# Performance work log

Measured on AMD Instinct MI355X. Metric: run time of the kernel, lower is better.

## Reference

```python
import jax, jax.numpy as jnp
import numpy as np

N_EMBD = 1024
N_HEADS = 16
HEAD_EMBD = N_EMBD // N_HEADS  # 64
TOTAL = N_HEADS * HEAD_EMBD


def setup_inputs() -> dict:
    key = jax.random.key(0)
    k_x, k_wqkv, k_bqkv, k_wo, k_bo = jax.random.split(key, 5)
    B, S = 2, 2048
    x = jax.random.normal(k_x, (B, S, N_EMBD), dtype=jnp.float32)
    # torch nn.Linear: weight (out, in), y = x @ W.T + b
    lim_qkv = 1.0 / np.sqrt(N_EMBD)
    W_qkv = jax.random.uniform(k_wqkv, (3 * TOTAL, N_EMBD), minval=-lim_qkv, maxval=lim_qkv, dtype=jnp.float32)
    b_qkv = jax.random.uniform(k_bqkv, (3 * TOTAL,), minval=-lim_qkv, maxval=lim_qkv, dtype=jnp.float32)
    lim_o = 1.0 / np.sqrt(TOTAL)
    W_out = jax.random.uniform(k_wo, (N_EMBD, TOTAL), minval=-lim_o, maxval=lim_o, dtype=jnp.float32)
    b_out = jax.random.uniform(k_bo, (N_EMBD,), minval=-lim_o, maxval=lim_o, dtype=jnp.float32)
    return {"x": x, "W_qkv": W_qkv, "b_qkv": b_qkv, "W_out": W_out, "b_out": b_out}


def reference(x, W_qkv, b_qkv, W_out, b_out):
    B, S, _ = x.shape
    qkv = x @ W_qkv.T + b_qkv  # (B, S, 3*H*E)
    # rearrange 'b s (t h e) -> t b h s e'
    qkv = qkv.reshape(B, S, 3, N_HEADS, HEAD_EMBD)
    q = jnp.transpose(qkv[:, :, 0], (0, 2, 1, 3))  # (B, H, S, E)
    k = jnp.transpose(qkv[:, :, 1], (0, 2, 1, 3))
    v = jnp.transpose(qkv[:, :, 2], (0, 2, 1, 3))
    scores = jnp.einsum('bhse,bhte->bhst', q, k) / jnp.sqrt(jnp.float32(HEAD_EMBD))
    # original: tril(scores) + triu(-10000, k=1) == strict-upper entries exactly -10000
    row = jnp.arange(S)[:, None]
    col = jnp.arange(S)[None, :]
    masked = jnp.where(col > row, jnp.float32(-10000.0), scores)
    attn = jax.nn.softmax(masked, axis=-1)  # (B, H, S, S)
    z = jnp.einsum('bhrc,bhce->bhre', attn, v)  # (B, H, S, E)
    z = jnp.transpose(z, (0, 2, 1, 3)).reshape(B, S, TOTAL)
    out = z @ W_out.T + b_out
    return (out, attn)
```

## Files before the change

### kernel.cpp

```cpp
#include <hip/hip_runtime.h>
#include <stdint.h>

typedef __attribute__((ext_vector_type(4))) float f32x4;
typedef __attribute__((ext_vector_type(8))) short short8v;
typedef __attribute__((ext_vector_type(4))) unsigned short ushort4v;

#define DEV __device__ __forceinline__
#define EXP2 __builtin_amdgcn_exp2f
#define WAITVM0 asm volatile("s_waitcnt vmcnt(0)" ::: "memory")
#define WAITVM2 asm volatile("s_waitcnt vmcnt(2)" ::: "memory")
#define WAITVM4 asm volatile("s_waitcnt vmcnt(4)" ::: "memory")
#define FENCE   asm volatile("" ::: "memory")
#define BARRIER __builtin_amdgcn_s_barrier()

DEV unsigned short f2bf(float x) {
    union { float f; uint32_t u; } v; v.f = x;
    uint32_t r = v.u + 0x7fffu + ((v.u >> 16) & 1u);
    return (unsigned short)(r >> 16);
}
DEV float bf2f(unsigned short h) {
    union { uint32_t u; float f; } v; v.u = ((uint32_t)h) << 16;
    return v.f;
}
DEV uint32_t cvtpk(float lo, float hi) {
    uint32_t r;
    asm("v_cvt_pk_bf16_f32 %0, %1, %2" : "=v"(r) : "v"(lo), "v"(hi));
    return r;
}
DEV f32x4 mfma16(short8v a, short8v b, f32x4 c) {
    return __builtin_amdgcn_mfma_f32_16x16x32_bf16(a, b, c, 0, 0, 0);
}
DEV void gload16(const unsigned short* g, unsigned short* l) {
    __builtin_amdgcn_global_load_lds(
        (const __attribute__((address_space(1))) unsigned int*)g,
        (__attribute__((address_space(3))) unsigned int*)l, 16, 0, 0);
}

__global__ void k_cvt3(const float* __restrict__ a, unsigned short* __restrict__ oa, int na4,
                       const float* __restrict__ b, unsigned short* __restrict__ ob, int nb4,
                       const float* __restrict__ c, unsigned short* __restrict__ oc, int nc4) {
    int i = blockIdx.x * blockDim.x + threadIdx.x;
    const float* in; unsigned short* out; int idx;
    if (i < na4) { in = a; out = oa; idx = i; }
    else if (i < na4 + nb4) { in = b; out = ob; idx = i - na4; }
    else { idx = i - na4 - nb4; if (idx >= nc4) return; in = c; out = oc; }
    f32x4 v = *(const f32x4*)(in + (size_t)idx * 4);
    ushort4v h;
#pragma unroll
    for (int j = 0; j < 4; ++j) h[j] = f2bf(v[j]);
    *(ushort4v*)(out + (size_t)idx * 4) = h;
}

template <int KDIM>
DEV void gemm_core(const unsigned short* __restrict__ APTR,
                   const unsigned short* __restrict__ BPTR,
                   f32x4 (&acc)[4][4]) {
    __shared__ __align__(16) unsigned short As[2][128 * 32], Bs[2][128 * 32];
    int tid = threadIdx.x, lane = tid & 63, w = tid >> 6;
    int bm = blockIdx.x, bn = blockIdx.y;
    int wr = (w >> 1) * 64, wc = (w & 1) * 64;
    int lrow = lane & 15, lseg = lane >> 4;
#pragma unroll
    for (int m = 0; m < 4; ++m)
#pragma unroll
        for (int n = 0; n < 4; ++n) acc[m][n] = (f32x4){0.f, 0.f, 0.f, 0.f};
    auto STAGE = [&](int buf, int k0) {
#pragma unroll
        for (int i = 0; i < 2; ++i) {
            int ch = i * 256 + tid;
            int row = ch >> 2, seg = ch & 3;
            gload16(APTR + (size_t)(bm * 128 + row) * KDIM + k0 + seg * 8,
                    &As[buf][(i * 256 + (tid & ~63)) * 8]);
            gload16(BPTR + (size_t)(bn * 128 + row) * KDIM + k0 + seg * 8,
                    &Bs[buf][(i * 256 + (tid & ~63)) * 8]);
        }
    };
    const int NT = KDIM / 32;
    STAGE(0, 0);
    for (int t = 0; t < NT; ++t) {
        if (t < NT - 1) { STAGE((t + 1) & 1, (t + 1) * 32); WAITVM4; } else WAITVM0;
        BARRIER;
        const unsigned short* as = As[t & 1];
        const unsigned short* bs = Bs[t & 1];
        short8v fa[4], fb[4];
#pragma unroll
        for (int m = 0; m < 4; ++m) {
            fa[m] = *(const short8v*)(as + (wr + m * 16 + lrow) * 32 + lseg * 8);
            fb[m] = *(const short8v*)(bs + (wc + m * 16 + lrow) * 32 + lseg * 8);
        }
#pragma unroll
        for (int m = 0; m < 4; ++m)
#pragma unroll
            for (int n = 0; n < 4; ++n)
                acc[m][n] = mfma16(fa[m], fb[n], acc[m][n]);
        FENCE; BARRIER;
    }
}

__global__ __launch_bounds__(256) void k_gemm_qkv(
    const unsigned short* __restrict__ XB, const unsigned short* __restrict__ WB,
    const float* __restrict__ BIAS, unsigned short* __restrict__ QKVB) {
    f32x4 acc[4][4];
    gemm_core<1024>(XB, WB, acc);
    int tid = threadIdx.x, lane = tid & 63, w = tid >> 6;
    int bm = blockIdx.x, bn = blockIdx.y;
    int wr = (w >> 1) * 64, wc = (w & 1) * 64;
    int lrow = lane & 15, lseg = lane >> 4;
    const int N = 3072;
#pragma unroll
    for (int n = 0; n < 4; ++n) {
        int col = bn * 128 + wc + n * 16 + lrow;
        float bv = BIAS[col];
#pragma unroll
        for (int m = 0; m < 4; ++m) {
            int row = bm * 128 + wr + m * 16 + lseg * 4;
#pragma unroll
            for (int i = 0; i < 4; ++i)
                QKVB[(size_t)(row + i) * N + col] = f2bf(acc[m][n][i] + bv);
        }
    }
}

__global__ __launch_bounds__(256) void k_gemm_out(
    const unsigned short* __restrict__ ZB, const unsigned short* __restrict__ WOB,
    const float* __restrict__ BIAS, float* __restrict__ OUT) {
    f32x4 acc[4][4];
    gemm_core<1024>(ZB, WOB, acc);
    int tid = threadIdx.x, lane = tid & 63, w = tid >> 6;
    int bm = blockIdx.x, bn = blockIdx.y;
    int wr = (w >> 1) * 64, wc = (w & 1) * 64;
    int lrow = lane & 15, lseg = lane >> 4;
    const int N = 1024;
#pragma unroll
    for (int n = 0; n < 4; ++n) {
        int col = bn * 128 + wc + n * 16 + lrow;
        float bv = BIAS[col];
#pragma unroll
        for (int m = 0; m < 4; ++m) {
            int row = bm * 128 + wr + m * 16 + lseg * 4;
#pragma unroll
            for (int i = 0; i < 4; ++i)
                OUT[(size_t)(row + i) * N + col] = acc[m][n][i] + bv;
        }
    }
}

__global__ void k_prep_v(const unsigned short* __restrict__ QKVB, unsigned short* __restrict__ VT) {
    __shared__ unsigned short vt[32][72];
    int bh = blockIdx.y, b = bh >> 4, h = bh & 15;
    int c0 = blockIdx.x * 32;
    int t = threadIdx.x;
    int c = t >> 3, e8 = (t & 7) * 8;
    *(short8v*)&vt[c][e8] =
        *(const short8v*)(QKVB + (size_t)(b * 2048 + c0 + c) * 3072 + 2048 + h * 64 + e8);
    __syncthreads();
    int e = t & 63, cg = t >> 6;
    unsigned short tmp[8];
#pragma unroll
    for (int i = 0; i < 8; ++i) tmp[i] = vt[cg * 8 + i][e];
    *(short8v*)(VT + ((size_t)bh * 64 + e) * 2048 + c0 + cg * 8) = *(short8v*)tmp;
}

__global__ __launch_bounds__(512) void k_attn(
    const unsigned short* __restrict__ QKVB, const unsigned short* __restrict__ VT,
    float* __restrict__ ATTN, unsigned short* __restrict__ Z) {
    __shared__ __align__(16) unsigned short KV[2][8192];
    __shared__ __align__(16) float Pl[8][16][68];

    const float SCALE = 0.18033688011112042f;
    int blk = blockIdx.x;
    int bh = blk & 31;
    int rtp = blk >> 5;
    int rt = (rtp < 8) ? (15 - rtp) : (rtp - 8);
    int b = bh >> 4, h = bh & 15;
    int tid = threadIdx.x, lane = tid & 63, w = tid >> 6;
    int lrow = lane & 15, lseg = lane >> 4;
    int r0 = rt * 128 + w * 16;
    int T = 2 * rt + 2;
    int Tw = (r0 >> 6) + 1;

    short8v qf[2];
    {
        const unsigned short* qp =
            QKVB + (size_t)(b * 2048 + r0 + lrow) * 3072 + h * 64 + lseg * 8;
#pragma unroll
        for (int kc = 0; kc < 2; ++kc) {
            short8v qr = *(const short8v*)(qp + kc * 32);
            short8v qs;
#pragma unroll
            for (int j = 0; j < 8; ++j)
                qs[j] = (short)f2bf(bf2f((unsigned short)qr[j]) * SCALE);
            qf[kc] = qs;
        }
    }

    auto STAGEKA = [&](int buf, int t) {
        const size_t kbase = ((size_t)b * 2048 + (size_t)t * 128) * 3072 + 1024 + h * 64;
#pragma unroll
        for (int i2 = 0; i2 < 2; ++i2) {
            int ch = i2 * 512 + tid;
            int c = ch >> 3, u = ch & 7, us = u ^ (c & 7);
            gload16(QKVB + kbase + (size_t)c * 3072 + us * 8,
                    &KV[buf][(i2 * 512 + (tid & ~63)) * 8]);
        }
    };
    float ls4[4] = {0.f, 0.f, 0.f, 0.f};
    int TA = rt + 1;
    STAGEKA(0, 0);
    for (int t = 0; t < TA; ++t) {
        if (t < TA - 1) { STAGEKA((t + 1) & 1, t + 1); WAITVM2; } else WAITVM0;
        BARRIER;
        const unsigned short* kb = KV[t & 1];
        f32x4 sc[8];
#pragma unroll
        for (int g = 0; g < 8; ++g) sc[g] = (f32x4){0.f, 0.f, 0.f, 0.f};
#pragma unroll
        for (int kc = 0; kc < 2; ++kc) {
            int uoff = (((kc * 4 + lseg) ^ (lrow & 7)) << 3);
#pragma unroll
            for (int g = 0; g < 8; ++g) {
                short8v kf = *(const short8v*)(kb + (g * 16 + lrow) * 64 + uoff);
                sc[g] = mfma16(qf[kc], kf, sc[g]);
            }
        }
        if (t < TA - 1) {
#pragma unroll
            for (int g = 0; g < 8; ++g)
#pragma unroll
                for (int i = 0; i < 4; ++i) ls4[i] += EXP2(sc[g][i]);
        } else {
            int c0 = t * 128;
#pragma unroll
            for (int g = 0; g < 8; ++g)
#pragma unroll
                for (int i = 0; i < 4; ++i) {
                    float sv = (c0 + g * 16 + lrow > r0 + lseg * 4 + i) ? -1e30f : sc[g][i];
                    ls4[i] += EXP2(sv);
                }
        }
        FENCE; BARRIER;
    }
#pragma unroll
    for (int off = 1; off < 16; off <<= 1)
#pragma unroll
        for (int i = 0; i < 4; ++i) ls4[i] += __shfl_xor(ls4[i], off, 64);
    float invl[4];
#pragma unroll
    for (int i = 0; i < 4; ++i) invl[i] = 1.0f / ls4[i];

    auto STAGEKB = [&](int buf, int t) {
        const size_t kbase = ((size_t)b * 2048 + (size_t)t * 64) * 3072 + 1024 + h * 64;
        int c = tid >> 3, u = tid & 7, us = u ^ (c & 7);
        gload16(QKVB + kbase + (size_t)c * 3072 + us * 8, &KV[buf][(tid & ~63) * 8]);
    };
    auto STAGEVB = [&](int buf, int t) {
        const size_t vbase = (size_t)bh * 64 * 2048 + (size_t)t * 64;
        int e = tid >> 3, u = tid & 7, us = u ^ (e & 7);
        gload16(VT + vbase + (size_t)e * 2048 + us * 8, &KV[buf][4096 + (tid & ~63) * 8]);
    };

    float* ab = ATTN + ((size_t)bh * 2048 + r0) * 2048;
    f32x4 zacc[4];
#pragma unroll
    for (int i = 0; i < 4; ++i) zacc[i] = (f32x4){0.f, 0.f, 0.f, 0.f};

    STAGEKB(0, 0); STAGEVB(0, 0);
    for (int t = 0; t < T; ++t) {
        if (t < T - 1) { STAGEKB((t + 1) & 1, t + 1); STAGEVB((t + 1) & 1, t + 1); WAITVM2; }
        else WAITVM0;
        BARRIER;
        if (t < Tw) {
            const unsigned short* kb = KV[t & 1];
            const unsigned short* vb = KV[t & 1] + 4096;
            int c0 = t * 64;
            f32x4 sc[4];
#pragma unroll
            for (int g = 0; g < 4; ++g) sc[g] = (f32x4){0.f, 0.f, 0.f, 0.f};
#pragma unroll
            for (int kc = 0; kc < 2; ++kc) {
                int uoff = (((kc * 4 + lseg) ^ (lrow & 7)) << 3);
#pragma unroll
                for (int g = 0; g < 4; ++g) {
                    short8v kf = *(const short8v*)(kb + (g * 16 + lrow) * 64 + uoff);
                    sc[g] = mfma16(qf[kc], kf, sc[g]);
                }
            }
            if (t < Tw - 1) {
#pragma unroll
                for (int g = 0; g < 4; ++g)
#pragma unroll
                    for (int i = 0; i < 4; ++i)
                        Pl[w][lseg * 4 + i][g * 16 + lrow] = EXP2(sc[g][i]) * invl[i];
            } else {
#pragma unroll
                for (int g = 0; g < 4; ++g)
#pragma unroll
                    for (int i = 0; i < 4; ++i) {
                        float sv = (c0 + g * 16 + lrow > r0 + lseg * 4 + i) ? -1e30f : sc[g][i];
                        Pl[w][lseg * 4 + i][g * 16 + lrow] = EXP2(sv) * invl[i];
                    }
            }
            short8v pf[2];
#pragma unroll
            for (int kc = 0; kc < 2; ++kc) {
                f32x4 p0 = *(const f32x4*)&Pl[w][lrow][kc * 32 + lseg * 8];
                f32x4 p1 = *(const f32x4*)&Pl[w][lrow][kc * 32 + lseg * 8 + 4];
                union { uint32_t u[4]; short8v s; } pu;
                pu.u[0] = cvtpk(p0[0], p0[1]);
                pu.u[1] = cvtpk(p0[2], p0[3]);
                pu.u[2] = cvtpk(p1[0], p1[1]);
                pu.u[3] = cvtpk(p1[2], p1[3]);
                pf[kc] = pu.s;
            }
#pragma unroll
            for (int kc = 0; kc < 2; ++kc) {
                int uoff = (((kc * 4 + lseg) ^ (lrow & 7)) << 3);
#pragma unroll
                for (int et = 0; et < 4; ++et) {
                    short8v vf = *(const short8v*)(vb + (et * 16 + lrow) * 64 + uoff);
                    zacc[et] = mfma16(pf[kc], vf, zacc[et]);
                }
            }
            {
                int row4 = lane >> 4, cq = lane & 15;
#pragma unroll
                for (int r4 = 0; r4 < 4; ++r4) {
                    int row = r4 * 4 + row4;
                    *(f32x4*)(ab + (size_t)row * 2048 + c0 + cq * 4) =
                        *(const f32x4*)(&Pl[w][row][cq * 4]);
                }
            }
        }
        FENCE; BARRIER;
    }

#pragma unroll
    for (int et = 0; et < 4; ++et)
#pragma unroll
        for (int i = 0; i < 4; ++i)
            Z[(size_t)(b * 2048 + r0 + lseg * 4 + i) * 1024 + h * 64 + et * 16 + lrow] =
                f2bf(zacc[et][i]);

    int czw = Tw * 64;
    const f32x4 zz = (f32x4){0.f, 0.f, 0.f, 0.f};
    for (int r = 0; r < 16; ++r) {
        float* rp = ab + (size_t)r * 2048;
        for (int c = czw + (lane << 2); c < 2048; c += 256)
            *(f32x4*)(rp + c) = zz;
    }
}

extern "C" void kernel_launch(void* const* d_in, const int* in_sizes, int n_in,
                              void* d_out, int out_size, void* d_ws, size_t ws_size,
                              hipStream_t stream) {
    const float* X    = (const float*)d_in[0];
    const float* Wqkv = (const float*)d_in[1];
    const float* Bqkv = (const float*)d_in[2];
    const float* Wout = (const float*)d_in[3];
    const float* Bout = (const float*)d_in[4];
    float* out  = (float*)d_out;
    float* attn = out + (size_t)4096 * 1024;

    char* ws = (char*)d_ws;
    unsigned short* QKVB = (unsigned short*)ws; ws += (size_t)4096 * 3072 * 2;
    unsigned short* VTp  = (unsigned short*)ws; ws += (size_t)32 * 64 * 2048 * 2;
    unsigned short* ZBp  = (unsigned short*)ws; ws += (size_t)4096 * 1024 * 2;
    unsigned short* XBp  = (unsigned short*)ws; ws += (size_t)4096 * 1024 * 2;
    unsigned short* WQBp = (unsigned short*)ws; ws += (size_t)3072 * 1024 * 2;
    unsigned short* WOBp = (unsigned short*)ws; ws += (size_t)1024 * 1024 * 2;

    const int na4 = 4096 * 1024 / 4, nb4 = 3072 * 1024 / 4, nc4 = 1024 * 1024 / 4;
    k_cvt3<<<(na4 + nb4 + nc4 + 255) / 256, 256, 0, stream>>>(
        X, XBp, na4, Wqkv, WQBp, nb4, Wout, WOBp, nc4);
    k_gemm_qkv<<<dim3(32, 24), 256, 0, stream>>>(XBp, WQBp, Bqkv, QKVB);
    k_prep_v<<<dim3(64, 32), 256, 0, stream>>>(QKVB, VTp);
    k_attn<<<512, 512, 0, stream>>>(QKVB, VTp, attn, ZBp);
    k_gemm_out<<<dim3(32, 8), 256, 0, stream>>>(ZBp, WOBp, Bout, out);
}
```

Baseline: 243.4 us.

## Specialize warps in pass A: half compute row sums, half zero-fill masked attention

During the first (row-sum) pass, warps 0-3 now each compute softmax denominators for 32 rows, reusing staged K tiles across two Q fragments. Warps 4-7 meanwhile write zeros to the fully masked upper-triangle region of the attention output, interleaved across the pass-A iterations. Reciprocal sums are shared through shared memory. The intent is to hide the large zero-fill store traffic behind pass-A compute instead of doing it at the end, at the cost of halving the MFMA warps in pass A. A launch-bounds occupancy hint is also added.

```diff
diff --git a/kernel.cpp b/kernel.cpp
--- a/kernel.cpp
+++ b/kernel.cpp
@@ -10,6 +10,7 @@
 #define WAITVM0 asm volatile("s_waitcnt vmcnt(0)" ::: "memory")
 #define WAITVM2 asm volatile("s_waitcnt vmcnt(2)" ::: "memory")
 #define WAITVM4 asm volatile("s_waitcnt vmcnt(4)" ::: "memory")
+#define WAITLGKM0 asm volatile("s_waitcnt lgkmcnt(0)" ::: "memory")
 #define FENCE   asm volatile("" ::: "memory")
 #define BARRIER __builtin_amdgcn_s_barrier()
 
@@ -161,11 +162,12 @@
     *(short8v*)(VT + ((size_t)bh * 64 + e) * 2048 + c0 + cg * 8) = *(short8v*)tmp;
 }
 
-__global__ __launch_bounds__(512) void k_attn(
+__global__ __launch_bounds__(512, 4) void k_attn(
     const unsigned short* __restrict__ QKVB, const unsigned short* __restrict__ VT,
     float* __restrict__ ATTN, unsigned short* __restrict__ Z) {
     __shared__ __align__(16) unsigned short KV[2][8192];
     __shared__ __align__(16) float Pl[8][16][68];
+    __shared__ float Rinv[128];
 
     const float SCALE = 0.18033688011112042f;
     int blk = blockIdx.x;
@@ -178,6 +180,7 @@
     int r0 = rt * 128 + w * 16;
     int T = 2 * rt + 2;
     int Tw = (r0 >> 6) + 1;
+    int TA = rt + 1;
 
     short8v qf[2];
     {
@@ -197,56 +200,100 @@
     auto STAGEKA = [&](int buf, int t) {
         const size_t kbase = ((size_t)b * 2048 + (size_t)t * 128) * 3072 + 1024 + h * 64;
 #pragma unroll
-        for (int i2 = 0; i2 < 2; ++i2) {
-            int ch = i2 * 512 + tid;
+        for (int i2 = 0; i2 < 4; ++i2) {
+            int ch = i2 * 256 + tid;
             int c = ch >> 3, u = ch & 7, us = u ^ (c & 7);
             gload16(QKVB + kbase + (size_t)c * 3072 + us * 8,
-                    &KV[buf][(i2 * 512 + (tid & ~63)) * 8]);
+                    &KV[buf][(i2 * 256 + (tid & ~63)) * 8]);
         }
     };
-    float ls4[4] = {0.f, 0.f, 0.f, 0.f};
-    int TA = rt + 1;
-    STAGEKA(0, 0);
-    for (int t = 0; t < TA; ++t) {
-        if (t < TA - 1) { STAGEKA((t + 1) & 1, t + 1); WAITVM2; } else WAITVM0;
-        BARRIER;
-        const unsigned short* kb = KV[t & 1];
-        f32x4 sc[8];
-#pragma unroll
-        for (int g = 0; g < 8; ++g) sc[g] = (f32x4){0.f, 0.f, 0.f, 0.f};
-#pragma unroll
-        for (int kc = 0; kc < 2; ++kc) {
-            int uoff = (((kc * 4 + lseg) ^ (lrow & 7)) << 3);
-#pragma unroll
-            for (int g = 0; g < 8; ++g) {
-                short8v kf = *(const short8v*)(kb + (g * 16 + lrow) * 64 + uoff);
-                sc[g] = mfma16(qf[kc], kf, sc[g]);
-            }
-        }
-        if (t < TA - 1) {
-#pragma unroll
-            for (int g = 0; g < 8; ++g)
-#pragma unroll
-                for (int i = 0; i < 4; ++i) ls4[i] += EXP2(sc[g][i]);
-        } else {
-            int c0 = t * 128;
-#pragma unroll
-            for (int g = 0; g < 8; ++g)
-#pragma unroll
-                for (int i = 0; i < 4; ++i) {
-                    float sv = (c0 + g * 16 + lrow > r0 + lseg * 4 + i) ? -1e30f : sc[g][i];
-                    ls4[i] += EXP2(sv);
+    const f32x4 zz = (f32x4){0.f, 0.f, 0.f, 0.f};
+
+    if (w < 4) {
+        int r0A = rt * 128 + w * 32;
+        short8v qa[2][2];
+#pragma unroll
+        for (int g2 = 0; g2 < 2; ++g2) {
+            const unsigned short* qp =
+                QKVB + (size_t)(b * 2048 + r0A + g2 * 16 + lrow) * 3072 + h * 64 + lseg * 8;
+#pragma unroll
+            for (int kc = 0; kc < 2; ++kc) {
+                short8v qr = *(const short8v*)(qp + kc * 32);
+                short8v qs;
+#pragma unroll
+                for (int j = 0; j < 8; ++j)
+                    qs[j] = (short)f2bf(bf2f((unsigned short)qr[j]) * SCALE);
+                qa[g2][kc] = qs;
+            }
+        }
+        float ls8[8] = {0.f, 0.f, 0.f, 0.f, 0.f, 0.f, 0.f, 0.f};
+        STAGEKA(0, 0);
+        for (int t = 0; t < TA; ++t) {
+            if (t < TA - 1) { STAGEKA((t + 1) & 1, t + 1); WAITVM4; } else WAITVM0;
+            BARRIER;
+            const unsigned short* kb = KV[t & 1];
+#pragma unroll
+            for (int g2 = 0; g2 < 2; ++g2) {
+                f32x4 sc[8];
+#pragma unroll
+                for (int g = 0; g < 8; ++g) sc[g] = zz;
+#pragma unroll
+                for (int kc = 0; kc < 2; ++kc) {
+                    int uoff = (((kc * 4 + lseg) ^ (lrow & 7)) << 3);
+#pragma unroll
+                    for (int g = 0; g < 8; ++g) {
+                        short8v kf = *(const short8v*)(kb + (g * 16 + lrow) * 64 + uoff);
+                        sc[g] = mfma16(qa[g2][kc], kf, sc[g]);
+                    }
                 }
-        }
-        FENCE; BARRIER;
-    }
-#pragma unroll
-    for (int off = 1; off < 16; off <<= 1)
-#pragma unroll
-        for (int i = 0; i < 4; ++i) ls4[i] += __shfl_xor(ls4[i], off, 64);
+                if (t < TA - 1) {
+#pragma unroll
+                    for (int g = 0; g < 8; ++g)
+#pragma unroll
+                        for (int i = 0; i < 4; ++i) ls8[g2 * 4 + i] += EXP2(sc[g][i]);
+                } else {
+                    int c0 = t * 128;
+#pragma unroll
+                    for (int g = 0; g < 8; ++g)
+#pragma unroll
+                        for (int i = 0; i < 4; ++i) {
+                            float sv = (c0 + g * 16 + lrow > r0A + g2 * 16 + lseg * 4 + i)
+                                           ? -1e30f : sc[g][i];
+                            ls8[g2 * 4 + i] += EXP2(sv);
+                        }
+                }
+            }
+            FENCE; BARRIER;
+        }
+#pragma unroll
+        for (int off = 1; off < 16; off <<= 1)
+#pragma unroll
+            for (int i = 0; i < 8; ++i) ls8[i] += __shfl_xor(ls8[i], off, 64);
+        if (lrow == 0) {
+#pragma unroll
+            for (int g2 = 0; g2 < 2; ++g2)
+#pragma unroll
+                for (int i = 0; i < 4; ++i)
+                    Rinv[w * 32 + g2 * 16 + lseg * 4 + i] = 1.0f / ls8[g2 * 4 + i];
+        }
+    } else {
+        int j = w - 4;
+        for (int t = 0; t < TA; ++t) {
+            BARRIER;
+            for (int rr = t; rr < 32; rr += TA) {
+                int grow = rt * 128 + j * 32 + rr;
+                int czw = ((grow >> 6) + 1) * 64;
+                float* rp = ATTN + ((size_t)bh * 2048 + grow) * 2048;
+                for (int c = czw + (lane << 2); c < 2048; c += 256)
+                    *(f32x4*)(rp + c) = zz;
+            }
+            FENCE; BARRIER;
+        }
+    }
+    WAITLGKM0; BARRIER;
     float invl[4];
 #pragma unroll
-    for (int i = 0; i < 4; ++i) invl[i] = 1.0f / ls4[i];
+    for (int i = 0; i < 4; ++i) invl[i] = Rinv[w * 16 + lseg * 4 + i];
 
     auto STAGEKB = [&](int buf, int t) {
         const size_t kbase = ((size_t)b * 2048 + (size_t)t * 64) * 3072 + 1024 + h * 64;
@@ -262,7 +309,7 @@
     float* ab = ATTN + ((size_t)bh * 2048 + r0) * 2048;
     f32x4 zacc[4];
 #pragma unroll
-    for (int i = 0; i < 4; ++i) zacc[i] = (f32x4){0.f, 0.f, 0.f, 0.f};
+    for (int i = 0; i < 4; ++i) zacc[i] = zz;
 
     STAGEKB(0, 0); STAGEVB(0, 0);
     for (int t = 0; t < T; ++t) {
@@ -275,7 +322,7 @@
             int c0 = t * 64;
             f32x4 sc[4];
 #pragma unroll
-            for (int g = 0; g < 4; ++g) sc[g] = (f32x4){0.f, 0.f, 0.f, 0.f};
+            for (int g = 0; g < 4; ++g) sc[g] = zz;
 #pragma unroll
             for (int kc = 0; kc < 2; ++kc) {
                 int uoff = (((kc * 4 + lseg) ^ (lrow & 7)) << 3);
@@ -340,14 +387,6 @@
         for (int i = 0; i < 4; ++i)
             Z[(size_t)(b * 2048 + r0 + lseg * 4 + i) * 1024 + h * 64 + et * 16 + lrow] =
                 f2bf(zacc[et][i]);
-
-    int czw = Tw * 64;
-    const f32x4 zz = (f32x4){0.f, 0.f, 0.f, 0.f};
-    for (int r = 0; r < 16; ++r) {
-        float* rp = ab + (size_t)r * 2048;
-        for (int c = czw + (lane << 2); c < 2048; c += 256)
-            *(f32x4*)(rp + c) = zz;
-    }
 }
 
 extern "C" void kernel_launch(void* const* d_in, const int* in_sizes, int n_in,
```

Result: slower. 271.4 us (+11.5%).

## Pack probability tile as bf16 pairs and cap registers for more occupancy

Applied to the files above, without the earlier changes.

The per-wave probability scratch tile now holds bf16 pairs packed into uint32 instead of fp32, which halves its shared-memory footprint. Lanes unpack the odd or even halves with masks and shifts, both to build the MFMA A fragment and to write the attention output. Pass A computes its 128-column tile in two halves of four groups to lower register pressure, and launch bounds request six waves per EU so more blocks fit on a CU. The cost is that the written attention probabilities are now rounded to bf16 rather than kept in fp32, plus some extra bit manipulation.

```diff
diff --git a/kernel.cpp b/kernel.cpp
--- a/kernel.cpp
+++ b/kernel.cpp
@@ -2,6 +2,7 @@
 #include <stdint.h>
 
 typedef __attribute__((ext_vector_type(4))) float f32x4;
+typedef __attribute__((ext_vector_type(4))) unsigned int uint4v;
 typedef __attribute__((ext_vector_type(8))) short short8v;
 typedef __attribute__((ext_vector_type(4))) unsigned short ushort4v;
 
@@ -161,11 +162,11 @@
     *(short8v*)(VT + ((size_t)bh * 64 + e) * 2048 + c0 + cg * 8) = *(short8v*)tmp;
 }
 
-__global__ __launch_bounds__(512) void k_attn(
+__global__ __launch_bounds__(512, 6) void k_attn(
     const unsigned short* __restrict__ QKVB, const unsigned short* __restrict__ VT,
     float* __restrict__ ATTN, unsigned short* __restrict__ Z) {
     __shared__ __align__(16) unsigned short KV[2][8192];
-    __shared__ __align__(16) float Pl[8][16][68];
+    __shared__ __align__(16) uint32_t Pl2[8][8][68];
 
     const float SCALE = 0.18033688011112042f;
     int blk = blockIdx.x;
@@ -211,32 +212,37 @@
         if (t < TA - 1) { STAGEKA((t + 1) & 1, t + 1); WAITVM2; } else WAITVM0;
         BARRIER;
         const unsigned short* kb = KV[t & 1];
-        f32x4 sc[8];
-#pragma unroll
-        for (int g = 0; g < 8; ++g) sc[g] = (f32x4){0.f, 0.f, 0.f, 0.f};
-#pragma unroll
-        for (int kc = 0; kc < 2; ++kc) {
-            int uoff = (((kc * 4 + lseg) ^ (lrow & 7)) << 3);
-#pragma unroll
-            for (int g = 0; g < 8; ++g) {
-                short8v kf = *(const short8v*)(kb + (g * 16 + lrow) * 64 + uoff);
-                sc[g] = mfma16(qf[kc], kf, sc[g]);
-            }
-        }
-        if (t < TA - 1) {
-#pragma unroll
-            for (int g = 0; g < 8; ++g)
-#pragma unroll
-                for (int i = 0; i < 4; ++i) ls4[i] += EXP2(sc[g][i]);
-        } else {
-            int c0 = t * 128;
-#pragma unroll
-            for (int g = 0; g < 8; ++g)
-#pragma unroll
-                for (int i = 0; i < 4; ++i) {
-                    float sv = (c0 + g * 16 + lrow > r0 + lseg * 4 + i) ? -1e30f : sc[g][i];
-                    ls4[i] += EXP2(sv);
-                }
+        int c0 = t * 128;
+#pragma unroll
+        for (int half = 0; half < 2; ++half) {
+            f32x4 sc[4];
+#pragma unroll
+            for (int g = 0; g < 4; ++g) sc[g] = (f32x4){0.f, 0.f, 0.f, 0.f};
+#pragma unroll
+            for (int kc = 0; kc < 2; ++kc) {
+                int uoff = (((kc * 4 + lseg) ^ (lrow & 7)) << 3);
+#pragma unroll
+                for (int g = 0; g < 4; ++g) {
+                    int gg = half * 4 + g;
+                    short8v kf = *(const short8v*)(kb + (gg * 16 + lrow) * 64 + uoff);
+                    sc[g] = mfma16(qf[kc], kf, sc[g]);
+                }
+            }
+            if (t < TA - 1) {
+#pragma unroll
+                for (int g = 0; g < 4; ++g)
+#pragma unroll
+                    for (int i = 0; i < 4; ++i) ls4[i] += EXP2(sc[g][i]);
+            } else {
+#pragma unroll
+                for (int g = 0; g < 4; ++g)
+#pragma unroll
+                    for (int i = 0; i < 4; ++i) {
+                        int gg = half * 4 + g;
+                        float sv = (c0 + gg * 16 + lrow > r0 + lseg * 4 + i) ? -1e30f : sc[g][i];
+                        ls4[i] += EXP2(sv);
+                    }
+            }
         }
         FENCE; BARRIER;
     }
@@ -287,38 +293,50 @@
             }
             if (t < Tw - 1) {
 #pragma unroll
-                for (int g = 0; g < 4; ++g)
-#pragma unroll
-                    for (int i = 0; i < 4; ++i)
-                        Pl[w][lseg * 4 + i][g * 16 + lrow] = EXP2(sc[g][i]) * invl[i];
+                for (int g = 0; g < 4; ++g) {
+                    float p0 = EXP2(sc[g][0]) * invl[0];
+                    float p1 = EXP2(sc[g][1]) * invl[1];
+                    float p2 = EXP2(sc[g][2]) * invl[2];
+                    float p3 = EXP2(sc[g][3]) * invl[3];
+                    Pl2[w][lseg * 2][g * 16 + lrow] = cvtpk(p0, p1);
+                    Pl2[w][lseg * 2 + 1][g * 16 + lrow] = cvtpk(p2, p3);
+                }
             } else {
 #pragma unroll
-                for (int g = 0; g < 4; ++g)
+                for (int g = 0; g < 4; ++g) {
+                    float p[4];
 #pragma unroll
                     for (int i = 0; i < 4; ++i) {
                         float sv = (c0 + g * 16 + lrow > r0 + lseg * 4 + i) ? -1e30f : sc[g][i];
-                        Pl[w][lseg * 4 + i][g * 16 + lrow] = EXP2(sv) * invl[i];
+                        p[i] = EXP2(sv) * invl[i];
                     }
-            }
-            short8v pf[2];
-#pragma unroll
-            for (int kc = 0; kc < 2; ++kc) {
-                f32x4 p0 = *(const f32x4*)&Pl[w][lrow][kc * 32 + lseg * 8];
-                f32x4 p1 = *(const f32x4*)&Pl[w][lrow][kc * 32 + lseg * 8 + 4];
-                union { uint32_t u[4]; short8v s; } pu;
-                pu.u[0] = cvtpk(p0[0], p0[1]);
-                pu.u[1] = cvtpk(p0[2], p0[3]);
-                pu.u[2] = cvtpk(p1[0], p1[1]);
-                pu.u[3] = cvtpk(p1[2], p1[3]);
-                pf[kc] = pu.s;
-            }
-#pragma unroll
-            for (int kc = 0; kc < 2; ++kc) {
-                int uoff = (((kc * 4 + lseg) ^ (lrow & 7)) << 3);
-#pragma unroll
-                for (int et = 0; et < 4; ++et) {
-                    short8v vf = *(const short8v*)(vb + (et * 16 + lrow) * 64 + uoff);
-                    zacc[et] = mfma16(pf[kc], vf, zacc[et]);
+                    Pl2[w][lseg * 2][g * 16 + lrow] = cvtpk(p[0], p[1]);
+                    Pl2[w][lseg * 2 + 1][g * 16 + lrow] = cvtpk(p[2], p[3]);
+                }
+            }
+            {
+                const uint32_t* prow = &Pl2[w][lrow >> 1][0];
+                uint32_t oddm = (lrow & 1) ? 0xFFFFFFFFu : 0u;
+#pragma unroll
+                for (int kc = 0; kc < 2; ++kc) {
+                    uint4v qa = *(const uint4v*)(prow + kc * 32 + lseg * 8);
+                    uint4v qb = *(const uint4v*)(prow + kc * 32 + lseg * 8 + 4);
+                    union { uint32_t u[4]; short8v s; } pu;
+#pragma unroll
+                    for (int w2 = 0; w2 < 2; ++w2) {
+                        uint32_t a0 = qa[2 * w2], a1 = qa[2 * w2 + 1];
+                        uint32_t b0 = qb[2 * w2], b1 = qb[2 * w2 + 1];
+                        pu.u[w2] = (oddm ? ((a0 >> 16) | (a1 & 0xFFFF0000u))
+                                         : ((a0 & 0xFFFFu) | (a1 << 16)));
+                        pu.u[w2 + 2] = (oddm ? ((b0 >> 16) | (b1 & 0xFFFF0000u))
+                                             : ((b0 & 0xFFFFu) | (b1 << 16)));
+                    }
+                    int uoff = (((kc * 4 + lseg) ^ (lrow & 7)) << 3);
+#pragma unroll
+                    for (int et = 0; et < 4; ++et) {
+                        short8v vf = *(const short8v*)(vb + (et * 16 + lrow) * 64 + uoff);
+                        zacc[et] = mfma16(pu.s, vf, zacc[et]);
+                    }
                 }
             }
             {
@@ -326,8 +344,16 @@
 #pragma unroll
                 for (int r4 = 0; r4 < 4; ++r4) {
                     int row = r4 * 4 + row4;
-                    *(f32x4*)(ab + (size_t)row * 2048 + c0 + cq * 4) =
-                        *(const f32x4*)(&Pl[w][row][cq * 4]);
+                    uint4v qv = *(const uint4v*)(&Pl2[w][row >> 1][cq * 4]);
+                    union { uint32_t u[4]; f32x4 f; } ov;
+                    if (row & 1) {
+#pragma unroll
+                        for (int k = 0; k < 4; ++k) ov.u[k] = qv[k] & 0xFFFF0000u;
+                    } else {
+#pragma unroll
+                        for (int k = 0; k < 4; ++k) ov.u[k] = qv[k] << 16;
+                    }
+                    *(f32x4*)(ab + (size_t)row * 2048 + c0 + cq * 4) = ov.f;
                 }
             }
         }
```

New measurement: 259.8 us. 6.7% more time.
